# Kernel optimization log

Measured on AMD Instinct MI355X. Metric: run time of the kernel, lower is better.

The kernel has to match this reference:

```python
import jax, jax.numpy as jnp
import numpy as np

N_DATA = 32768
N_CHK = 32768
N = N_DATA + N_CHK          # 65536 nodes
E = 524288                  # edges (before self-loops)
F_IN = 10                   # node_feature_dim
HID = 128                   # hidden_dim
HEADS = 4
C = HID // HEADS            # 32 per-head channels
L = 4                       # num_gnn_layers
EPS_LN = 1e-5


def layer_norm(x, g, b):
    mu = x.mean(-1, keepdims=True)
    var = ((x - mu) ** 2).mean(-1, keepdims=True)
    return (x - mu) * jax.lax.rsqrt(var + EPS_LN) * g + b


def mlp3(x, W1, b1, W2, b2, W3, b3):
    h = jax.nn.relu(x @ W1 + b1)
    h = jax.nn.relu(h @ W2 + b2)
    return h @ W3 + b3


def setup_inputs() -> dict:
    key = jax.random.key(0)
    ks = jax.random.split(key, 32)
    s = 0.02
    inp = {
        'node_features': jax.random.normal(ks[0], (N, F_IN), jnp.float32),
        'edge_index': jax.random.randint(ks[1], (2, E), 0, N, dtype=jnp.int64),
        # node embedding: Linear(F_IN,HID) + LayerNorm
        'W_emb': s * jax.random.normal(ks[2], (F_IN, HID), jnp.float32),
        'b_emb': jnp.zeros((HID,), jnp.float32),
        'ln0_g': jnp.ones((HID,), jnp.float32),
        'ln0_b': jnp.zeros((HID,), jnp.float32),
        # L GATConv layers (stacked): lin weight, att_src/att_dst, bias, post-LN
        'Wg': s * jax.random.normal(ks[3], (L, HID, HID), jnp.float32),
        'att_s': s * jax.random.normal(ks[4], (L, HEADS, C), jnp.float32),
        'att_d': s * jax.random.normal(ks[5], (L, HEADS, C), jnp.float32),
        'bg': jnp.zeros((L, HID), jnp.float32),
        'lng': jnp.ones((L, HID), jnp.float32),
        'lnb': jnp.zeros((L, HID), jnp.float32),
        # policy net
        'pW1': s * jax.random.normal(ks[6], (HID, HID), jnp.float32),
        'pb1': jnp.zeros((HID,), jnp.float32),
        'pW2': s * jax.random.normal(ks[7], (HID, HID // 2), jnp.float32),
        'pb2': jnp.zeros((HID // 2,), jnp.float32),
        'pW3': s * jax.random.normal(ks[8], (HID // 2, 2), jnp.float32),
        'pb3': jnp.zeros((2,), jnp.float32),
        # value net
        'vW1': s * jax.random.normal(ks[9], (HID, HID), jnp.float32),
        'vb1': jnp.zeros((HID,), jnp.float32),
        'vW2': s * jax.random.normal(ks[10], (HID, HID // 2), jnp.float32),
        'vb2': jnp.zeros((HID // 2,), jnp.float32),
        'vW3': s * jax.random.normal(ks[11], (HID // 2, 1), jnp.float32),
        'vb3': jnp.zeros((1,), jnp.float32),
    }
    return inp


def reference(node_features, edge_index, W_emb, b_emb, ln0_g, ln0_b,
              Wg, att_s, att_d, bg, lng, lnb,
              pW1, pb1, pW2, pb2, pW3, pb3,
              vW1, vb1, vW2, vb2, vW3, vb3):
    n = node_features.shape[0]
    # PyG GATConv adds self-loops by default
    loops = jnp.arange(n, dtype=edge_index.dtype)
    ei = jnp.concatenate([edge_index, jnp.stack([loops, loops])], axis=1)
    src, dst = ei[0], ei[1]

    # node embedding (dropout is identity in eval)
    x = jax.nn.relu(layer_norm(node_features @ W_emb + b_emb, ln0_g, ln0_b))

    for l in range(L):
        h = (x @ Wg[l]).reshape(n, HEADS, C)                       # [N,H,C]
        a_s = jnp.einsum('nhc,hc->nh', h, att_s[l])                # [N,H]
        a_d = jnp.einsum('nhc,hc->nh', h, att_d[l])
        alpha = jax.nn.leaky_relu(a_s[src] + a_d[dst], 0.2)        # [E+N,H]
        # segment softmax over destination node per head
        m = jax.ops.segment_max(alpha, dst, num_segments=n)
        alpha = jnp.exp(alpha - m[dst])
        denom = jax.ops.segment_sum(alpha, dst, num_segments=n)
        alpha = alpha / (denom[dst] + 1e-16)
        out = jax.ops.segment_sum(alpha[:, :, None] * h[src], dst,
                                  num_segments=n)                  # [N,H,C]
        out = out.reshape(n, HID) + bg[l]
        x = layer_norm(x + jax.nn.relu(out), lng[l], lnb[l])

    logits = mlp3(x[:N_DATA], pW1, pb1, pW2, pb2, pW3, pb3)        # [N_DATA,2]
    pooled = x.mean(axis=0, keepdims=True)                         # [1,HID]
    value = mlp3(pooled, vW1, vb1, vW2, vb2, vW3, vb3)             # [1,1]
    return logits, value
```

## Files before the change

kernel.cpp:

```cpp
#include <hip/hip_runtime.h>

#define NNODES 65536
#define NDATA  32768
#define HID    128
#define HEADS  4
#define CHANS  32
#define LAYERS 4

using bf16x8 = __attribute__((ext_vector_type(8))) short;
using f32x4  = __attribute__((ext_vector_type(4))) float;

__device__ __forceinline__ float wave_reduce_sum(float v) {
#pragma unroll
    for (int m = 1; m < 64; m <<= 1) v += __shfl_xor(v, m, 64);
    return v;
}

__device__ __forceinline__ int wave_reduce_sum_i(int v) {
#pragma unroll
    for (int m = 1; m < 64; m <<= 1) v += __shfl_xor(v, m, 64);
    return v;
}

__device__ __forceinline__ unsigned short bf16_rne(float f) {
    unsigned u = __float_as_uint(f);
    return (unsigned short)((u + 0x7fffu + ((u >> 16) & 1u)) >> 16);
}
__device__ __forceinline__ float bf2f(unsigned short u) {
    return __uint_as_float((unsigned)u << 16);
}

__device__ __forceinline__ void gload_lds16(const unsigned short* g, unsigned short* l) {
    __builtin_amdgcn_global_load_lds(
        (const __attribute__((address_space(1))) void*)g,
        (__attribute__((address_space(3))) void*)l, 16, 0, 0);
}

__global__ void hist_kernel(const int* __restrict__ ei, int* __restrict__ deg, int Eo) {
    int e = blockIdx.x * 256 + threadIdx.x;
    if (e >= Eo) return;
    atomicAdd(&deg[ei[Eo + e]], 1);
}

__global__ void scan1(const int* __restrict__ deg, int* __restrict__ offs, int* __restrict__ bsum) {
    __shared__ int s[256];
    int t = threadIdx.x, b = blockIdx.x;
    int v = deg[b * 256 + t] + 1;
    s[t] = v;
    __syncthreads();
    for (int off = 1; off < 256; off <<= 1) {
        int add = (t >= off) ? s[t - off] : 0;
        __syncthreads();
        s[t] += add;
        __syncthreads();
    }
    offs[b * 256 + t] = s[t] - v;
    if (t == 255) bsum[b] = s[255];
}

__global__ void scan3(int* __restrict__ offs, const int* __restrict__ bsum,
                      int* __restrict__ cursor, int Eo) {
    __shared__ int ws[4];
    int b = blockIdx.x, t = threadIdx.x;
    int v = (t < b) ? bsum[t] : 0;
    v = wave_reduce_sum_i(v);
    if ((t & 63) == 0) ws[t >> 6] = v;
    __syncthreads();
    int base = ws[0] + ws[1] + ws[2] + ws[3];
    int i = b * 256 + t;
    int o = offs[i] + base;
    offs[i] = o;
    cursor[i] = o;
    if (i == 0) offs[NNODES] = Eo + NNODES;
}

__global__ void fill_kernel(const int* __restrict__ ei, int* __restrict__ cursor,
                            int* __restrict__ col, int Eo) {
    int e = blockIdx.x * 256 + threadIdx.x;
    int Etot = Eo + NNODES;
    if (e >= Etot) return;
    int src, dst;
    if (e < Eo) { src = ei[e]; dst = ei[Eo + e]; }
    else        { src = dst = e - Eo; }
    int pos = atomicAdd(&cursor[dst], 1);
    col[pos] = src;
}

__global__ __launch_bounds__(256) void prep_embed(
    const float* __restrict__ feat, const float* __restrict__ W_emb,
    const float* __restrict__ b_emb, const float* __restrict__ ln0g,
    const float* __restrict__ ln0b, unsigned short* __restrict__ xh,
    const float* __restrict__ Wg, const float* __restrict__ attS,
    const float* __restrict__ attD,
    const float* __restrict__ pW1, const float* __restrict__ pW2,
    const float* __restrict__ vW1, const float* __restrict__ vW2,
    unsigned short* __restrict__ wh, unsigned short* __restrict__ wl,
    unsigned short* __restrict__ w1h, unsigned short* __restrict__ w1l,
    unsigned short* __restrict__ w2h, unsigned short* __restrict__ w2l,
    float* __restrict__ w1t, float* __restrict__ w2t)
{
    if (blockIdx.x < NNODES / 4) {
        int node = blockIdx.x * 4 + (threadIdx.x >> 6);
        int lane = threadIdx.x & 63;
        float f[10];
#pragma unroll
        for (int i = 0; i < 10; i++) f[i] = feat[node * 10 + i];
        int c0 = 2 * lane, c1 = c0 + 1;
        float v0 = b_emb[c0], v1 = b_emb[c1];
#pragma unroll
        for (int i = 0; i < 10; i++) {
            v0 = fmaf(f[i], W_emb[i * HID + c0], v0);
            v1 = fmaf(f[i], W_emb[i * HID + c1], v1);
        }
        float mu = wave_reduce_sum(v0 + v1) * (1.f / 128.f);
        float e0 = v0 - mu, e1 = v1 - mu;
        float var = wave_reduce_sum(e0 * e0 + e1 * e1) * (1.f / 128.f);
        float r = 1.f / sqrtf(var + 1e-5f);
        float r0 = fmaxf(e0 * r * ln0g[c0] + ln0b[c0], 0.f);
        float r1 = fmaxf(e1 * r * ln0g[c1] + ln0b[c1], 0.f);
        *(unsigned*)(xh + (size_t)node * HID + c0) =
            (unsigned)bf16_rne(r0) | ((unsigned)bf16_rne(r1) << 16);
        return;
    }
    int id = (blockIdx.x - NNODES / 4) * 256 + threadIdx.x;
    if (id < 4 * 144 * 128) {
        int l = id / (144 * 128);
        int rem = id % (144 * 128);
        int n = rem / 128, k = rem % 128;
        const float* W = Wg + (size_t)l * HID * HID;
        float v = 0.f;
        if (n < 128) {
            v = W[k * HID + n];
        } else if (n < 136) {
            int h = (n - 128) & 3;
            const float* av = ((n - 128) < 4 ? attS : attD) + l * HID + h * CHANS;
            for (int c = 0; c < CHANS; c++) v += W[k * HID + h * CHANS + c] * av[c];
        }
        unsigned short hh = bf16_rne(v);
        int t = n >> 4, bcol = n & 15;
        int ks = k >> 5, kq = (k >> 3) & 3, e = k & 7;
        size_t o = (size_t)l * (144 * 128) + (size_t)(((t * 4 + ks) * 64) + (kq * 16 + bcol)) * 8 + e;
        wh[o] = hh;
        wl[o] = bf16_rne(v - bf2f(hh));
        return;
    }
    id -= 4 * 144 * 128;
    if (id < 24576) {
        int n, k;
        float v;
        unsigned short *dh, *dl;
        if (id < 16384) {
            n = id / 128; k = id % 128;
            v = pW1[k * 128 + n];
            dh = w1h; dl = w1l;
        } else {
            int j = id - 16384;
            n = j / 128; k = j % 128;
            v = pW2[k * 64 + n];
            dh = w2h; dl = w2l;
        }
        unsigned short hh = bf16_rne(v);
        int t = n >> 4, bcol = n & 15;
        int ks = k >> 5, kq = (k >> 3) & 3, e = k & 7;
        size_t o = (size_t)(((t * 4 + ks) * 64) + (kq * 16 + bcol)) * 8 + e;
        dh[o] = hh;
        dl[o] = bf16_rne(v - bf2f(hh));
        return;
    }
    id -= 24576;
    if (id < 16384) {
        int t = id >> 7, k = id & 127;
        w1t[t * 128 + k] = vW1[k * 128 + t];
    } else if (id < 24576) {
        int j = id - 16384;
        int t = j >> 7, k = j & 127;
        w2t[t * 128 + k] = vW2[k * 64 + t];
    }
}

template <int NT, int EPI>
__global__ __launch_bounds__(512, 4) void mfma_gemm(
    const unsigned short* __restrict__ Ah,
    const unsigned short* __restrict__ Bh, const unsigned short* __restrict__ Bl,
    const float* __restrict__ bias,
    unsigned short* __restrict__ outH,
    float* __restrict__ a_s, float* __restrict__ a_d,
    const float* __restrict__ wfin, const float* __restrict__ bfin,
    float* __restrict__ outF)
{
    __shared__ unsigned short lds[NT * 4096];

    int tid = threadIdx.x;
    int wid = tid >> 6, l = tid & 63;
    int row = blockIdx.x * 128 + wid * 16 + (l & 15);
    int kg = (l >> 4) * 8;

    for (int c = wid; c < 8 * NT; c += 8) {
        int fr = c >> 1, lo = c & 1;
        const unsigned short* src = (lo ? Bl : Bh) + ((size_t)fr << 9) + ((unsigned)l << 3);
        gload_lds16(src, &lds[(size_t)c << 9]);
    }

    const unsigned short* arh = Ah + (size_t)row * 128 + kg;
    bf16x8 afh[4];
#pragma unroll
    for (int ks = 0; ks < 4; ks++) afh[ks] = *(const bf16x8*)(arh + ks * 32);

    f32x4 acc[NT];
#pragma unroll
    for (int t = 0; t < NT; t++) acc[t] = (f32x4){0.f, 0.f, 0.f, 0.f};

    __syncthreads();

#pragma unroll
    for (int ks = 0; ks < 4; ks++) {
#pragma unroll
        for (int t = 0; t < NT; t++) {
            const unsigned short* bp = &lds[(((t * 4 + ks) << 1) << 9) + (l << 3)];
            bf16x8 bh  = *(const bf16x8*)bp;
            bf16x8 blo = *(const bf16x8*)(bp + 512);
            acc[t] = __builtin_amdgcn_mfma_f32_16x16x32_bf16(afh[ks], bh,  acc[t], 0, 0, 0);
            acc[t] = __builtin_amdgcn_mfma_f32_16x16x32_bf16(afh[ks], blo, acc[t], 0, 0, 0);
        }
    }

    int ecol = l & 15;
    int er0 = blockIdx.x * 128 + wid * 16 + ((l >> 4) << 2);

    if constexpr (EPI == 0) {
#pragma unroll
        for (int t = 0; t < 8; t++)
#pragma unroll
            for (int j = 0; j < 4; j++)
                outH[(size_t)(er0 + j) * 128 + t * 16 + ecol] = bf16_rne(acc[t][j]);
#pragma unroll
        for (int j = 0; j < 4; j++) {
            float v = acc[8][j];
            if (ecol < 4)      a_s[(er0 + j) * 4 + ecol] = v;
            else if (ecol < 8) a_d[(er0 + j) * 4 + (ecol - 4)] = v;
        }
    } else if constexpr (EPI == 1) {
#pragma unroll
        for (int t = 0; t < NT; t++)
#pragma unroll
            for (int j = 0; j < 4; j++) {
                float v = fmaxf(acc[t][j] + bias[t * 16 + ecol], 0.f);
                outH[(size_t)(er0 + j) * 128 + t * 16 + ecol] = bf16_rne(v);
            }
    } else {
        float p0[4], p1[4];
#pragma unroll
        for (int j = 0; j < 4; j++) { p0[j] = 0.f; p1[j] = 0.f; }
#pragma unroll
        for (int t = 0; t < NT; t++) {
            int cc = t * 16 + ecol;
            float w0 = wfin[cc * 2 + 0], w1 = wfin[cc * 2 + 1];
#pragma unroll
            for (int j = 0; j < 4; j++) {
                float v = fmaxf(acc[t][j] + bias[cc], 0.f);
                p0[j] = fmaf(v, w0, p0[j]);
                p1[j] = fmaf(v, w1, p1[j]);
            }
        }
#pragma unroll
        for (int m = 1; m < 16; m <<= 1)
#pragma unroll
            for (int j = 0; j < 4; j++) {
                p0[j] += __shfl_xor(p0[j], m, 64);
                p1[j] += __shfl_xor(p1[j], m, 64);
            }
        if (ecol == 0) {
            float b0 = bfin[0], b1 = bfin[1];
#pragma unroll
            for (int j = 0; j < 4; j++) {
                outF[(er0 + j) * 2 + 0] = p0[j] + b0;
                outF[(er0 + j) * 2 + 1] = p1[j] + b1;
            }
        }
    }
}

__global__ __launch_bounds__(256, 8) void gat_agg(
    const unsigned short* __restrict__ hb, const float* __restrict__ a_s,
    const float* __restrict__ a_d, const int* __restrict__ offs,
    const int* __restrict__ col, const float* __restrict__ bgl,
    const float* __restrict__ gl, const float* __restrict__ bl,
    unsigned short* __restrict__ xh)
{
    __shared__ int2 whs[4][4][64];
    int wv = threadIdx.x >> 6;
    int lane = threadIdx.x & 63;
    int node = blockIdx.x * 4 + wv;
    int s = offs[node], e = offs[node + 1];
    int deg = e - s;
    float4 ad = *(const float4*)(a_d + (size_t)node * 4);

    int c0 = 2 * lane, c1 = 2 * lane + 1;
    int head = lane >> 4;
    float acc0 = 0.f, acc1 = 0.f;
    float den = 1e-16f;

    if (deg <= 64) {
        int src = 0;
        float e0 = 0.f, e1 = 0.f, e2 = 0.f, e3 = 0.f;
        if (lane < deg) {
            src = col[s + lane];
            float4 as = *(const float4*)(a_s + (size_t)src * 4);
            float s0 = as.x + ad.x; s0 = fmaxf(s0, 0.2f * s0);
            float s1 = as.y + ad.y; s1 = fmaxf(s1, 0.2f * s1);
            float s2 = as.z + ad.z; s2 = fmaxf(s2, 0.2f * s2);
            float s3 = as.w + ad.w; s3 = fmaxf(s3, 0.2f * s3);
            e0 = __expf(s0); e1 = __expf(s1); e2 = __expf(s2); e3 = __expf(s3);
        }
        whs[wv][0][lane] = make_int2(__float_as_int(e0), src);
        whs[wv][1][lane] = make_int2(__float_as_int(e1), src);
        whs[wv][2][lane] = make_int2(__float_as_int(e2), src);
        whs[wv][3][lane] = make_int2(__float_as_int(e3), src);
        const int2* wrow = &whs[wv][head][0];
        int dg8 = (deg + 7) & ~7;
        for (int j = 0; j < dg8; j += 8) {
            int2 q[8];
#pragma unroll
            for (int u = 0; u < 8; u++) q[u] = wrow[j + u];
            unsigned hv[8];
#pragma unroll
            for (int u = 0; u < 8; u++)
                hv[u] = *(const unsigned*)(hb + (((unsigned)q[u].y << 7) + (unsigned)c0));
#pragma unroll
            for (int u = 0; u < 8; u++) {
                float w = __int_as_float(q[u].x);
                den += w;
                acc0 = fmaf(w, __uint_as_float(hv[u] << 16), acc0);
                acc1 = fmaf(w, __uint_as_float(hv[u] & 0xffff0000u), acc1);
            }
        }
    } else {
        for (int j = s; j < e; j++) {
            int src = col[j];
            float4 as = *(const float4*)(a_s + (size_t)src * 4);
            float sh = (head == 0) ? (as.x + ad.x) : (head == 1) ? (as.y + ad.y)
                     : (head == 2) ? (as.z + ad.z) : (as.w + ad.w);
            sh = fmaxf(sh, 0.2f * sh);
            float wj = __expf(sh);
            den += wj;
            unsigned hv = *(const unsigned*)(hb + (((unsigned)src << 7) + (unsigned)c0));
            acc0 = fmaf(wj, __uint_as_float(hv << 16), acc0);
            acc1 = fmaf(wj, __uint_as_float(hv & 0xffff0000u), acc1);
        }
    }
    float inv = 1.f / den;
    acc0 *= inv;
    acc1 *= inv;

    float o0 = fmaxf(acc0 + bgl[c0], 0.f);
    float o1 = fmaxf(acc1 + bgl[c1], 0.f);
    size_t xi = (size_t)node * HID;
    unsigned ph = *(const unsigned*)(xh + xi + c0);
    float t0 = __uint_as_float(ph << 16) + o0;
    float t1 = __uint_as_float(ph & 0xffff0000u) + o1;
    float mu = wave_reduce_sum(t0 + t1) * (1.f / 128.f);
    float e0 = t0 - mu, e1 = t1 - mu;
    float var = wave_reduce_sum(e0 * e0 + e1 * e1) * (1.f / 128.f);
    float r = 1.f / sqrtf(var + 1e-5f);
    float r0 = e0 * r * gl[c0] + bl[c0];
    float r1 = e1 * r * gl[c1] + bl[c1];
    *(unsigned*)(xh + xi + c0) = (unsigned)bf16_rne(r0) | ((unsigned)bf16_rne(r1) << 16);
}

__global__ void pool_sum(const unsigned short* __restrict__ xh, float* __restrict__ partial) {
    int t = threadIdx.x;
    int base = blockIdx.x * 256;
    float s = 0.f;
    for (int i = 0; i < 256; i++)
        s += bf2f(xh[(size_t)(base + i) * HID + t]);
    partial[blockIdx.x * 128 + t] = s;
}

__global__ void value_mlp(const float* __restrict__ partial,
                          const float* __restrict__ w1t, const float* __restrict__ b1,
                          const float* __restrict__ w2t, const float* __restrict__ b2,
                          const float* __restrict__ W3, const float* __restrict__ b3,
                          float* __restrict__ out)
{
    __shared__ float p[128], h1[128], h2[64];
    int t = threadIdx.x;
    float s = 0.f;
    for (int i = 0; i < 256; i++) s += partial[i * 128 + t];
    p[t] = s * (1.f / (float)NNODES);
    __syncthreads();
    float a = b1[t];
    const float4* wr = (const float4*)(w1t + (size_t)t * 128);
#pragma unroll
    for (int k4 = 0; k4 < 32; k4++) {
        float4 w = wr[k4];
        a += p[4 * k4] * w.x + p[4 * k4 + 1] * w.y + p[4 * k4 + 2] * w.z + p[4 * k4 + 3] * w.w;
    }
    h1[t] = fmaxf(a, 0.f);
    __syncthreads();
    if (t < 64) {
        float a2 = b2[t];
        const float4* wr2 = (const float4*)(w2t + (size_t)t * 128);
#pragma unroll
        for (int k4 = 0; k4 < 32; k4++) {
            float4 w = wr2[k4];
            a2 += h1[4 * k4] * w.x + h1[4 * k4 + 1] * w.y + h1[4 * k4 + 2] * w.z + h1[4 * k4 + 3] * w.w;
        }
        h2[t] = fmaxf(a2, 0.f);
    }
    __syncthreads();
    if (t == 0) {
        float v = b3[0];
        for (int k = 0; k < 64; k++) v = fmaf(h2[k], W3[k], v);
        out[NDATA * 2] = v;
    }
}

extern "C" void kernel_launch(void* const* d_in, const int* in_sizes, int n_in,
                              void* d_out, int out_size, void* d_ws, size_t ws_size,
                              hipStream_t stream)
{
    const float* feat  = (const float*)d_in[0];
    const int*   ei    = (const int*)d_in[1];
    const float* W_emb = (const float*)d_in[2];
    const float* b_emb = (const float*)d_in[3];
    const float* ln0g  = (const float*)d_in[4];
    const float* ln0b  = (const float*)d_in[5];
    const float* Wg    = (const float*)d_in[6];
    const float* att_s = (const float*)d_in[7];
    const float* att_d = (const float*)d_in[8];
    const float* bg    = (const float*)d_in[9];
    const float* lng   = (const float*)d_in[10];
    const float* lnb   = (const float*)d_in[11];
    const float* pW1 = (const float*)d_in[12]; const float* pb1 = (const float*)d_in[13];
    const float* pW2 = (const float*)d_in[14]; const float* pb2 = (const float*)d_in[15];
    const float* pW3 = (const float*)d_in[16]; const float* pb3 = (const float*)d_in[17];
    const float* vW1 = (const float*)d_in[18]; const float* vb1 = (const float*)d_in[19];
    const float* vW2 = (const float*)d_in[20]; const float* vb2 = (const float*)d_in[21];
    const float* vW3 = (const float*)d_in[22]; const float* vb3 = (const float*)d_in[23];
    float* out = (float*)d_out;
    int Eo = in_sizes[1] / 2;

    unsigned short* xh = (unsigned short*)d_ws;
    unsigned short* hb = xh + (size_t)NNODES * HID;
    float* a_s = (float*)(hb + (size_t)NNODES * HID);
    float* a_d = a_s + NNODES * HEADS;
    unsigned short* wgt_h = (unsigned short*)(a_d + NNODES * HEADS);
    unsigned short* wgt_l = wgt_h + 4 * 144 * 128;
    unsigned short* pw1h  = wgt_l + 4 * 144 * 128;
    unsigned short* pw1l  = pw1h + 128 * 128;
    unsigned short* pw2h  = pw1l + 128 * 128;
    unsigned short* pw2l  = pw2h + 64 * 128;
    float* w1t  = (float*)(pw2l + 64 * 128);
    float* w2t  = w1t + 128 * 128;
    float* partial = w2t + 64 * 128;
    int* deg    = (int*)(partial + 256 * 128);
    int* offs   = deg + NNODES;
    int* cursor = offs + NNODES + 2;
    int* bsum   = cursor + NNODES;
    int* col    = bsum + 256;
    unsigned short* ph1h = hb;

    prep_embed<<<NNODES / 4 + 480, 256, 0, stream>>>(
        feat, W_emb, b_emb, ln0g, ln0b, xh,
        Wg, att_s, att_d, pW1, pW2, vW1, vW2,
        wgt_h, wgt_l, pw1h, pw1l, pw2h, pw2l, w1t, w2t);

    hipMemsetAsync(deg, 0, (size_t)NNODES * 4, stream);
    hist_kernel<<<(Eo + 255) / 256, 256, 0, stream>>>(ei, deg, Eo);
    scan1<<<256, 256, 0, stream>>>(deg, offs, bsum);
    scan3<<<256, 256, 0, stream>>>(offs, bsum, cursor, Eo);
    fill_kernel<<<(Eo + NNODES + 255) / 256, 256, 0, stream>>>(ei, cursor, col, Eo);

    for (int l = 0; l < LAYERS; l++) {
        mfma_gemm<9, 0><<<NNODES / 128, 512, 0, stream>>>(
            xh, wgt_h + (size_t)l * 144 * 128, wgt_l + (size_t)l * 144 * 128,
            nullptr, hb, a_s, a_d, nullptr, nullptr, nullptr);
        gat_agg<<<NNODES / 4, 256, 0, stream>>>(
            hb, a_s, a_d, offs, col, bg + l * HID, lng + l * HID, lnb + l * HID, xh);
    }

    mfma_gemm<8, 1><<<NDATA / 128, 512, 0, stream>>>(
        xh, pw1h, pw1l, pb1, ph1h, nullptr, nullptr, nullptr, nullptr, nullptr);
    mfma_gemm<4, 2><<<NDATA / 128, 512, 0, stream>>>(
        ph1h, pw2h, pw2l, pb2, nullptr, nullptr, nullptr, pW3, pb3, out);

    pool_sum<<<256, 128, 0, stream>>>(xh, partial);
    value_mlp<<<1, 128, 0, stream>>>(partial, w1t, vb1, w2t, vb2, vW3, vb3, out);
}
```

Measured before the change: 317.3 us.

## Fuse policy MLP GEMMs through LDS and retile GAT linear GEMM to 2x5 waves

The two policy-head GEMMs merge into one kernel that keeps the hidden activations in shared memory, so they no longer go through global memory and one launch is saved. The per-layer GAT projection GEMM is retiled so each wave computes 32 rows by 5 column tiles instead of 16 rows by 9. This reuses each B fragment read from LDS across two row tiles. The 2x5 split leaves one redundant padded tile per wave, and the fused policy kernel's larger LDS footprint may reduce occupancy.

```diff
diff --git a/kernel.cpp b/kernel.cpp
--- a/kernel.cpp
+++ b/kernel.cpp
@@ -178,44 +178,128 @@
     }
 }
 
-template <int NT, int EPI>
-__global__ __launch_bounds__(512, 4) void mfma_gemm(
+__global__ __launch_bounds__(512, 4) void gemm_gat(
     const unsigned short* __restrict__ Ah,
     const unsigned short* __restrict__ Bh, const unsigned short* __restrict__ Bl,
-    const float* __restrict__ bias,
-    unsigned short* __restrict__ outH,
-    float* __restrict__ a_s, float* __restrict__ a_d,
-    const float* __restrict__ wfin, const float* __restrict__ bfin,
-    float* __restrict__ outF)
+    unsigned short* __restrict__ hb, float* __restrict__ a_s, float* __restrict__ a_d)
 {
-    __shared__ unsigned short lds[NT * 4096];
+    __shared__ unsigned short lds[9 * 4096];
 
     int tid = threadIdx.x;
     int wid = tid >> 6, l = tid & 63;
-    int row = blockIdx.x * 128 + wid * 16 + (l & 15);
-    int kg = (l >> 4) * 8;
-
-    for (int c = wid; c < 8 * NT; c += 8) {
+    int wr = wid >> 1, wc = wid & 1;
+    int cb = wc * 4;
+
+    for (int c = wid; c < 72; c += 8) {
         int fr = c >> 1, lo = c & 1;
         const unsigned short* src = (lo ? Bl : Bh) + ((size_t)fr << 9) + ((unsigned)l << 3);
         gload_lds16(src, &lds[(size_t)c << 9]);
     }
 
-    const unsigned short* arh = Ah + (size_t)row * 128 + kg;
+    int row0 = blockIdx.x * 128 + wr * 32 + (l & 15);
+    int kg = (l >> 4) * 8;
+    bf16x8 afh[2][4];
+#pragma unroll
+    for (int rt = 0; rt < 2; rt++) {
+        const unsigned short* ar = Ah + (size_t)(row0 + rt * 16) * 128 + kg;
+#pragma unroll
+        for (int ks = 0; ks < 4; ks++) afh[rt][ks] = *(const bf16x8*)(ar + ks * 32);
+    }
+
+    f32x4 acc[2][5];
+#pragma unroll
+    for (int rt = 0; rt < 2; rt++)
+#pragma unroll
+        for (int ct = 0; ct < 5; ct++) acc[rt][ct] = (f32x4){0.f, 0.f, 0.f, 0.f};
+
+    __syncthreads();
+
+#pragma unroll
+    for (int ks = 0; ks < 4; ks++) {
+#pragma unroll
+        for (int ct = 0; ct < 5; ct++) {
+            int t = cb + ct;
+            const unsigned short* bp = &lds[(((t * 4 + ks) << 1) << 9) + (l << 3)];
+            bf16x8 bh  = *(const bf16x8*)bp;
+            bf16x8 blo = *(const bf16x8*)(bp + 512);
+#pragma unroll
+            for (int rt = 0; rt < 2; rt++) {
+                acc[rt][ct] = __builtin_amdgcn_mfma_f32_16x16x32_bf16(afh[rt][ks], bh,  acc[rt][ct], 0, 0, 0);
+                acc[rt][ct] = __builtin_amdgcn_mfma_f32_16x16x32_bf16(afh[rt][ks], blo, acc[rt][ct], 0, 0, 0);
+            }
+        }
+    }
+
+    int ecol = l & 15;
+    int rbase = blockIdx.x * 128 + wr * 32 + ((l >> 4) << 2);
+#pragma unroll
+    for (int ct = 0; ct < 5; ct++) {
+        int t = cb + ct;
+        if (t < 8) {
+#pragma unroll
+            for (int rt = 0; rt < 2; rt++)
+#pragma unroll
+                for (int j = 0; j < 4; j++)
+                    hb[(size_t)(rbase + rt * 16 + j) * 128 + t * 16 + ecol] = bf16_rne(acc[rt][ct][j]);
+        } else {
+#pragma unroll
+            for (int rt = 0; rt < 2; rt++)
+#pragma unroll
+                for (int j = 0; j < 4; j++) {
+                    float v = acc[rt][ct][j];
+                    int rr = rbase + rt * 16 + j;
+                    if (ecol < 4)      a_s[rr * 4 + ecol] = v;
+                    else if (ecol < 8) a_d[rr * 4 + (ecol - 4)] = v;
+                }
+        }
+    }
+}
+
+__global__ __launch_bounds__(512, 2) void policy_fused(
+    const unsigned short* __restrict__ Ah,
+    const unsigned short* __restrict__ B1h, const unsigned short* __restrict__ B1l,
+    const float* __restrict__ b1,
+    const unsigned short* __restrict__ B2h, const unsigned short* __restrict__ B2l,
+    const float* __restrict__ b2,
+    const float* __restrict__ wfin, const float* __restrict__ bfin,
+    float* __restrict__ out)
+{
+    __shared__ unsigned short lds[96 * 512 + 128 * 136];
+    unsigned short* ph1 = &lds[96 * 512];
+
+    int tid = threadIdx.x;
+    int wid = tid >> 6, l = tid & 63;
+
+    for (int c = wid; c < 96; c += 8) {
+        const unsigned short* src;
+        if (c < 64) {
+            int fr = c >> 1, lo = c & 1;
+            src = (lo ? B1l : B1h) + ((size_t)fr << 9) + ((unsigned)l << 3);
+        } else {
+            int cc = c - 64;
+            int fr = cc >> 1, lo = cc & 1;
+            src = (lo ? B2l : B2h) + ((size_t)fr << 9) + ((unsigned)l << 3);
+        }
+        gload_lds16(src, &lds[(size_t)c << 9]);
+    }
+
+    int row = blockIdx.x * 128 + wid * 16 + (l & 15);
+    int kg = (l >> 4) * 8;
+    const unsigned short* ar = Ah + (size_t)row * 128 + kg;
     bf16x8 afh[4];
 #pragma unroll
-    for (int ks = 0; ks < 4; ks++) afh[ks] = *(const bf16x8*)(arh + ks * 32);
-
-    f32x4 acc[NT];
-#pragma unroll
-    for (int t = 0; t < NT; t++) acc[t] = (f32x4){0.f, 0.f, 0.f, 0.f};
+    for (int ks = 0; ks < 4; ks++) afh[ks] = *(const bf16x8*)(ar + ks * 32);
+
+    f32x4 acc[8];
+#pragma unroll
+    for (int t = 0; t < 8; t++) acc[t] = (f32x4){0.f, 0.f, 0.f, 0.f};
 
     __syncthreads();
 
 #pragma unroll
     for (int ks = 0; ks < 4; ks++) {
 #pragma unroll
-        for (int t = 0; t < NT; t++) {
+        for (int t = 0; t < 8; t++) {
             const unsigned short* bp = &lds[(((t * 4 + ks) << 1) << 9) + (l << 3)];
             bf16x8 bh  = *(const bf16x8*)bp;
             bf16x8 blo = *(const bf16x8*)(bp + 512);
@@ -225,57 +309,65 @@
     }
 
     int ecol = l & 15;
-    int er0 = blockIdx.x * 128 + wid * 16 + ((l >> 4) << 2);
-
-    if constexpr (EPI == 0) {
-#pragma unroll
-        for (int t = 0; t < 8; t++)
-#pragma unroll
-            for (int j = 0; j < 4; j++)
-                outH[(size_t)(er0 + j) * 128 + t * 16 + ecol] = bf16_rne(acc[t][j]);
+    int lr0 = wid * 16 + ((l >> 4) << 2);
+#pragma unroll
+    for (int t = 0; t < 8; t++)
 #pragma unroll
         for (int j = 0; j < 4; j++) {
-            float v = acc[8][j];
-            if (ecol < 4)      a_s[(er0 + j) * 4 + ecol] = v;
-            else if (ecol < 8) a_d[(er0 + j) * 4 + (ecol - 4)] = v;
-        }
-    } else if constexpr (EPI == 1) {
-#pragma unroll
-        for (int t = 0; t < NT; t++)
-#pragma unroll
-            for (int j = 0; j < 4; j++) {
-                float v = fmaxf(acc[t][j] + bias[t * 16 + ecol], 0.f);
-                outH[(size_t)(er0 + j) * 128 + t * 16 + ecol] = bf16_rne(v);
-            }
-    } else {
-        float p0[4], p1[4];
-#pragma unroll
-        for (int j = 0; j < 4; j++) { p0[j] = 0.f; p1[j] = 0.f; }
-#pragma unroll
-        for (int t = 0; t < NT; t++) {
-            int cc = t * 16 + ecol;
-            float w0 = wfin[cc * 2 + 0], w1 = wfin[cc * 2 + 1];
-#pragma unroll
-            for (int j = 0; j < 4; j++) {
-                float v = fmaxf(acc[t][j] + bias[cc], 0.f);
-                p0[j] = fmaf(v, w0, p0[j]);
-                p1[j] = fmaf(v, w1, p1[j]);
-            }
-        }
-#pragma unroll
-        for (int m = 1; m < 16; m <<= 1)
-#pragma unroll
-            for (int j = 0; j < 4; j++) {
-                p0[j] += __shfl_xor(p0[j], m, 64);
-                p1[j] += __shfl_xor(p1[j], m, 64);
-            }
-        if (ecol == 0) {
-            float b0 = bfin[0], b1 = bfin[1];
-#pragma unroll
-            for (int j = 0; j < 4; j++) {
-                outF[(er0 + j) * 2 + 0] = p0[j] + b0;
-                outF[(er0 + j) * 2 + 1] = p1[j] + b1;
-            }
+            float v = fmaxf(acc[t][j] + b1[t * 16 + ecol], 0.f);
+            ph1[(lr0 + j) * 136 + t * 16 + ecol] = bf16_rne(v);
+        }
+
+    int lrow = wid * 16 + (l & 15);
+    bf16x8 af2[4];
+#pragma unroll
+    for (int ks = 0; ks < 4; ks++)
+        af2[ks] = *(const bf16x8*)&ph1[lrow * 136 + kg + ks * 32];
+
+    f32x4 acc2[4];
+#pragma unroll
+    for (int t = 0; t < 4; t++) acc2[t] = (f32x4){0.f, 0.f, 0.f, 0.f};
+
+#pragma unroll
+    for (int ks = 0; ks < 4; ks++) {
+#pragma unroll
+        for (int t = 0; t < 4; t++) {
+            const unsigned short* bp = &lds[(size_t)(64 + ((t * 4 + ks) << 1)) * 512 + (l << 3)];
+            bf16x8 bh  = *(const bf16x8*)bp;
+            bf16x8 blo = *(const bf16x8*)(bp + 512);
+            acc2[t] = __builtin_amdgcn_mfma_f32_16x16x32_bf16(af2[ks], bh,  acc2[t], 0, 0, 0);
+            acc2[t] = __builtin_amdgcn_mfma_f32_16x16x32_bf16(af2[ks], blo, acc2[t], 0, 0, 0);
+        }
+    }
+
+    float p0[4], p1[4];
+#pragma unroll
+    for (int j = 0; j < 4; j++) { p0[j] = 0.f; p1[j] = 0.f; }
+#pragma unroll
+    for (int t = 0; t < 4; t++) {
+        int cc = t * 16 + ecol;
+        float w0 = wfin[cc * 2 + 0], w1 = wfin[cc * 2 + 1];
+#pragma unroll
+        for (int j = 0; j < 4; j++) {
+            float v = fmaxf(acc2[t][j] + b2[cc], 0.f);
+            p0[j] = fmaf(v, w0, p0[j]);
+            p1[j] = fmaf(v, w1, p1[j]);
+        }
+    }
+#pragma unroll
+    for (int m = 1; m < 16; m <<= 1)
+#pragma unroll
+        for (int j = 0; j < 4; j++) {
+            p0[j] += __shfl_xor(p0[j], m, 64);
+            p1[j] += __shfl_xor(p1[j], m, 64);
+        }
+    if (ecol == 0) {
+        int er0 = blockIdx.x * 128 + lr0;
+        float bb0 = bfin[0], bb1 = bfin[1];
+#pragma unroll
+        for (int j = 0; j < 4; j++) {
+            out[(er0 + j) * 2 + 0] = p0[j] + bb0;
+            out[(er0 + j) * 2 + 1] = p1[j] + bb1;
         }
     }
 }
@@ -458,7 +550,6 @@
     int* cursor = offs + NNODES + 2;
     int* bsum   = cursor + NNODES;
     int* col    = bsum + 256;
-    unsigned short* ph1h = hb;
 
     prep_embed<<<NNODES / 4 + 480, 256, 0, stream>>>(
         feat, W_emb, b_emb, ln0g, ln0b, xh,
@@ -472,17 +563,15 @@
     fill_kernel<<<(Eo + NNODES + 255) / 256, 256, 0, stream>>>(ei, cursor, col, Eo);
 
     for (int l = 0; l < LAYERS; l++) {
-        mfma_gemm<9, 0><<<NNODES / 128, 512, 0, stream>>>(
+        gemm_gat<<<NNODES / 128, 512, 0, stream>>>(
             xh, wgt_h + (size_t)l * 144 * 128, wgt_l + (size_t)l * 144 * 128,
-            nullptr, hb, a_s, a_d, nullptr, nullptr, nullptr);
+            hb, a_s, a_d);
         gat_agg<<<NNODES / 4, 256, 0, stream>>>(
             hb, a_s, a_d, offs, col, bg + l * HID, lng + l * HID, lnb + l * HID, xh);
     }
 
-    mfma_gemm<8, 1><<<NDATA / 128, 512, 0, stream>>>(
-        xh, pw1h, pw1l, pb1, ph1h, nullptr, nullptr, nullptr, nullptr, nullptr);
-    mfma_gemm<4, 2><<<NDATA / 128, 512, 0, stream>>>(
-        ph1h, pw2h, pw2l, pb2, nullptr, nullptr, nullptr, pW3, pb3, out);
+    policy_fused<<<NDATA / 128, 512, 0, stream>>>(
+        xh, pw1h, pw1l, pb1, pw2h, pw2l, pb2, pW3, pb3, out);
 
     pool_sum<<<256, 128, 0, stream>>>(xh, partial);
     value_mlp<<<1, 128, 0, stream>>>(partial, w1t, vb1, w2t, vb2, vW3, vb3, out);
```

Measured after the change: 318.5 us. Within noise of the previous version (+0.4%).
